# Kernel optimization log

Hardware: AMD Instinct MI355X
Metric: run time of the kernel (lower is better)

Reference implementation:

```python
import jax, jax.numpy as jnp
import numpy as np

B, T, I, H = 32, 1024, 512, 512


def _uniform(key, shape, stdv):
    return jax.random.uniform(key, shape, jnp.float32, -stdv, stdv)


def setup_inputs() -> dict:
    key = jax.random.key(0)
    ks = jax.random.split(key, 13)
    stdv = 1.0 / np.sqrt(H)
    return {
        "z": jax.random.normal(ks[0], (B, T, I, 2), jnp.float32),
        "W_zi": _uniform(ks[1], (I, H, 2), stdv), "W_hi": _uniform(ks[2], (H, H, 2), stdv), "b_i": _uniform(ks[3], (H,), stdv),
        "W_zf": _uniform(ks[4], (I, H, 2), stdv), "W_hf": _uniform(ks[5], (H, H, 2), stdv), "b_f": _uniform(ks[6], (H,), stdv),
        "W_zc": _uniform(ks[7], (I, H, 2), stdv), "W_hc": _uniform(ks[8], (H, H, 2), stdv), "b_c": _uniform(ks[9], (H, 2), stdv),
        "W_zo": _uniform(ks[10], (I, H, 2), stdv), "W_ho": _uniform(ks[11], (H, H, 2), stdv), "b_o": _uniform(ks[12], (H,), stdv),
    }


def complex_tanh(zr, zi):
    mag = jnp.maximum(jnp.sqrt(zr * zr + zi * zi + 1e-14), 1e-8)
    t = jnp.tanh(mag)
    return t * (zr / mag), t * (zi / mag)


def reference(z, W_zi, W_hi, b_i, W_zf, W_hf, b_f, W_zc, W_hc, b_c, W_zo, W_ho, b_o):
    zr, zi = z[..., 0], z[..., 1]  # (B,T,I)

    def in_proj_real(Wz):  # real part of complex matmul z @ Wz
        return jnp.einsum('bti,ih->bth', zr, Wz[..., 0]) - jnp.einsum('bti,ih->bth', zi, Wz[..., 1])

    xi = in_proj_real(W_zi)
    xf = in_proj_real(W_zf)
    xo = in_proj_real(W_zo)
    xcr = in_proj_real(W_zc)
    xci = jnp.einsum('bti,ih->bth', zi, W_zc[..., 0]) + jnp.einsum('bti,ih->bth', zr, W_zc[..., 1])

    # time-major for scan: (T,B,H)
    xs = tuple(jnp.swapaxes(a, 0, 1) for a in (xi, xf, xo, xcr, xci))

    def step(carry, x):
        h_r, h_i, c_r, c_i = carry
        xi_t, xf_t, xo_t, xcr_t, xci_t = x
        i_t = jax.nn.sigmoid(xi_t + h_r @ W_hi[..., 0] - h_i @ W_hi[..., 1] + b_i)
        f_t = jax.nn.sigmoid(xf_t + h_r @ W_hf[..., 0] - h_i @ W_hf[..., 1] + b_f)
        o_t = jax.nn.sigmoid(xo_t + h_r @ W_ho[..., 0] - h_i @ W_ho[..., 1] + b_o)
        cr = xcr_t + h_r @ W_hc[..., 0] - h_i @ W_hc[..., 1] + b_c[..., 0]
        ci = xci_t + h_i @ W_hc[..., 0] + h_r @ W_hc[..., 1] + b_c[..., 1]
        ctr, cti = complex_tanh(cr, ci)
        c_r = f_t * c_r + i_t * ctr
        c_i = f_t * c_i + i_t * cti
        hr, hi = complex_tanh(c_r, c_i)
        h_r = o_t * hr
        h_i = o_t * hi
        return (h_r, h_i, c_r, c_i), jnp.stack((h_r, h_i), axis=-1)

    zero = jnp.zeros((z.shape[0], W_hi.shape[0]), z.dtype)
    (h_r, h_i, c_r, c_i), hs = jax.lax.scan(step, (zero, zero, zero, zero), xs)
    hidden_seq = jnp.swapaxes(hs, 0, 1)  # (B,T,H,2)
    h_t = jnp.stack((h_r, h_i), axis=-1)
    c_t = jnp.stack((c_r, c_i), axis=-1)
    return hidden_seq, (h_t, c_t)
```

## Files before the change

### kernel.cpp

```cpp
#include <hip/hip_runtime.h>


#define B_ 32
#define T_ 1024
#define Hd 512
#define Kd 1024
#define Nd 2560
#define Md 32768
#define HS_ELEMS 33554432ull

typedef __attribute__((ext_vector_type(8))) short bf16x8;
typedef __attribute__((ext_vector_type(4))) float f32x4;

__device__ __forceinline__ unsigned short f_bf(float f) {
  unsigned int x; __builtin_memcpy(&x, &f, 4);
  unsigned int r = (x + 0x7FFFu + ((x >> 16) & 1u)) >> 16;
  return (unsigned short)r;
}
__device__ __forceinline__ float bf_f(unsigned short u) {
  unsigned int i = ((unsigned int)u) << 16; float f; __builtin_memcpy(&f, &i, 4); return f;
}
__device__ __forceinline__ float fsig(float x) { return 1.0f / (1.0f + __expf(-x)); }
__device__ __forceinline__ void ctanh_(float zr, float zi, float& tr, float& ti) {
  float m2 = zr * zr + zi * zi + 1e-14f;
  float mag = __fsqrt_rn(m2);
  float e = __expf(2.0f * mag);
  float th = 1.0f - 2.0f / (e + 1.0f);
  float s = th / mag;
  tr = zr * s; ti = zi * s;
}

__device__ __forceinline__ void gl16(const unsigned short* g, unsigned short* l) {
  __builtin_amdgcn_global_load_lds(
      (const __attribute__((address_space(1))) void*)g,
      (__attribute__((address_space(3))) void*)l, 16, 0, 0);
}

__device__ __forceinline__ unsigned int ald(const unsigned int* p) {
  return __hip_atomic_load(p, __ATOMIC_RELAXED, __HIP_MEMORY_SCOPE_AGENT);
}
__device__ __forceinline__ void ast(unsigned int* p, unsigned int v) {
  __hip_atomic_store(p, v, __ATOMIC_RELAXED, __HIP_MEMORY_SCOPE_AGENT);
}

__global__ void build_weights(const float* Wzi, const float* Whi, const float* bi,
                              const float* Wzf, const float* Whf, const float* bfv,
                              const float* Wzc, const float* Whc, const float* bc,
                              const float* Wzo, const float* Who, const float* bo,
                              unsigned short* WzT, unsigned short* WhT, float* bcomb) {
  int n = blockIdx.x;
  int slab = n / 80, wi = n % 80, g = wi / 16, hh = slab * 16 + (wi & 15);
  const float *Wz, *Wh;
  if (g == 0)      { Wz = Wzi; Wh = Whi; }
  else if (g == 1) { Wz = Wzf; Wh = Whf; }
  else if (g == 2) { Wz = Wzo; Wh = Who; }
  else             { Wz = Wzc; Wh = Whc; }
  int q0, q1; float s0, s1;
  if (g < 4) { q0 = 0; s0 = 1.f; q1 = 1; s1 = -1.f; }
  else       { q0 = 1; s0 = 1.f; q1 = 0; s1 =  1.f; }
  for (int k = threadIdx.x; k < Kd; k += 256) {
    int j = k >> 1, p = k & 1;
    int q = p ? q1 : q0; float sg = p ? s1 : s0;
    WzT[(size_t)n * Kd + k] = f_bf(sg * Wz[(j * Hd + hh) * 2 + q]);
    WhT[(size_t)n * Kd + k] = f_bf(sg * Wh[(j * Hd + hh) * 2 + q]);
  }
  if (threadIdx.x == 0) {
    float bv;
    if (g == 0) bv = bi[hh]; else if (g == 1) bv = bfv[hh];
    else if (g == 2) bv = bo[hh];
    else if (g == 3) bv = bc[2 * hh]; else bv = bc[2 * hh + 1];
    bcomb[n] = bv;
  }
}

__global__ void cvt_z(const float4* __restrict__ z, ushort4* __restrict__ Z2) {
  for (size_t i = (size_t)blockIdx.x * 256 + threadIdx.x; i < 8388608ull; i += 8192ull * 256) {
    float4 v = z[i];
    ushort4 o;
    o.x = f_bf(v.x); o.y = f_bf(v.y); o.z = f_bf(v.z); o.w = f_bf(v.w);
    Z2[i] = o;
  }
}

__global__ __launch_bounds__(256) void gemm_x(const unsigned short* __restrict__ Z2,
                                              const unsigned short* __restrict__ WT,
                                              unsigned short* __restrict__ X) {
  __shared__ unsigned short As[128 * 64];
  __shared__ unsigned short Bs[128 * 64];
  int tid = threadIdx.x, lane = tid & 63, wv = tid >> 6;
  int bid = blockIdx.x;
  int mb = bid / (Nd / 128), nb = bid % (Nd / 128);
  size_t m0 = (size_t)mb * 128, n0 = (size_t)nb * 128;
  int wr = wv >> 1, wc = wv & 1;
  int l15 = lane & 15, kg = lane >> 4;
  int lrow = tid >> 3;
  int lcol = (tid & 7) * 8;
  f32x4 acc[4][4] = {};
  for (int k0 = 0; k0 < Kd; k0 += 64) {
    __syncthreads();
#pragma unroll
    for (int c = 0; c < 4; ++c) {
      gl16(Z2 + (m0 + c * 32 + lrow) * Kd + k0 + lcol,
           As + (size_t)c * 2048 + wv * 512);
      gl16(WT + (n0 + c * 32 + lrow) * Kd + k0 + lcol,
           Bs + (size_t)c * 2048 + wv * 512);
    }
    __syncthreads();
#pragma unroll
    for (int ks = 0; ks < 2; ++ks) {
      int kk = ks * 32 + kg * 8;
      bf16x8 a[4], b[4];
#pragma unroll
      for (int i = 0; i < 4; ++i)
        a[i] = *reinterpret_cast<const bf16x8*>(&As[(wr * 64 + i * 16 + l15) * 64 + kk]);
#pragma unroll
      for (int j = 0; j < 4; ++j)
        b[j] = *reinterpret_cast<const bf16x8*>(&Bs[(wc * 64 + j * 16 + l15) * 64 + kk]);
#pragma unroll
      for (int i = 0; i < 4; ++i)
#pragma unroll
        for (int j = 0; j < 4; ++j)
          acc[i][j] = __builtin_amdgcn_mfma_f32_16x16x32_bf16(a[i], b[j], acc[i][j], 0, 0, 0);
    }
  }
#pragma unroll
  for (int i = 0; i < 4; ++i)
#pragma unroll
    for (int j = 0; j < 4; ++j) {
      size_t gm = m0 + wr * 64 + i * 16 + kg * 4;
      size_t gn = n0 + wc * 64 + j * 16 + l15;
#pragma unroll
      for (int r = 0; r < 4; ++r)
        X[(gm + r) * Nd + gn] = f_bf(acc[i][j][r]);
    }
}

#define CHUNK 8
#define STEPB (Nd * 2)
__global__ __launch_bounds__(512) void lstm_all(
    const unsigned short* __restrict__ WhT, const unsigned short* __restrict__ X,
    const float* __restrict__ bcomb, unsigned short* __restrict__ hb,
    int* __restrict__ flags, float* __restrict__ out) {
  __shared__ unsigned short Xs[2][CHUNK * STEPB / 2];
  __shared__ float xch[8][5][256];
  const int s = blockIdx.x;
  const int tid = threadIdx.x;
  const int wv = tid >> 6, lane = tid & 63;
  const int kh = wv >> 1, mh = wv & 1;
  const int l15 = lane & 15, kg = lane >> 4;
  const int cb = tid >> 4;
  const int ch = tid & 15;
  const int hh = s * 16 + ch;

  auto stage = [&](int tbase, int buf) {
#pragma unroll
    for (int j = 0; j < 5; ++j) {
      unsigned int P = (unsigned int)(wv * 5 + j) * 1024u + (unsigned int)lane * 16u;
      unsigned int st = P / STEPB, r = P % STEPB;
      unsigned int b = r / 160u, rem = r % 160u;
      gl16(X + ((size_t)b * T_ + (tbase + st)) * Nd + s * 80 + rem / 2,
           &Xs[buf][(size_t)(wv * 5 + j) * 512]);
    }
  };
  stage(0, 0);

  bf16x8 w[5][8];
#pragma unroll
  for (int g = 0; g < 5; ++g)
#pragma unroll
    for (int ks = 0; ks < 8; ++ks)
      w[g][ks] = *reinterpret_cast<const bf16x8*>(
          &WhT[(size_t)(s * 80 + g * 16 + l15) * Kd + kh * 256 + ks * 32 + kg * 8]);

  float bias[5];
#pragma unroll
  for (int g = 0; g < 5; ++g) bias[g] = bcomb[s * 80 + g * 16 + ch];
  float cr = 0.f, ci = 0.f;

  ast((unsigned int*)hb + (size_t)cb * 512 + s * 16 + ch, 0u);
  asm volatile("s_waitcnt vmcnt(0)" ::: "memory");
  __syncthreads();
  if (tid == 0) ast((unsigned int*)&flags[s], 1u);

  const int fidx = kh * 8 + (lane & 7);
  const int mb = cb >> 4;
  const int xidx = ((cb & 15) >> 2) * 64 + ch * 4 + (cb & 3);

  for (int t = 0; t < T_; ++t) {
    const unsigned int need = (unsigned int)(t + 1);
    while (true) {
      unsigned int v = ald((const unsigned int*)&flags[fidx]);
      if (__all(v >= need)) break;
    }
    asm volatile("" ::: "memory");

    const unsigned short* hin = hb + (size_t)(t % 3) * 32768;
    unsigned long long hpa = (unsigned long long)(
        hin + (size_t)(mh * 16 + l15) * Kd + kh * 256 + kg * 8);
    bf16x8 a[8];
#define HL(i, off) asm volatile("global_load_dwordx4 %0, %1, off offset:" #off " sc0 sc1" \
                                 : "=v"(a[i]) : "v"(hpa) : "memory")
    HL(0, 0); HL(1, 64); HL(2, 128); HL(3, 192);
    HL(4, 256); HL(5, 320); HL(6, 384); HL(7, 448);
#undef HL
    asm volatile("s_waitcnt vmcnt(0)" ::: "memory");
    __builtin_amdgcn_sched_barrier(0);

    if ((t & (CHUNK - 1)) == 0 && t + CHUNK < T_)
      stage(t + CHUNK, ((t >> 3) + 1) & 1);

    f32x4 acc[5] = {};
#pragma unroll
    for (int ks = 0; ks < 8; ++ks)
#pragma unroll
      for (int g = 0; g < 5; ++g)
        acc[g] = __builtin_amdgcn_mfma_f32_16x16x32_bf16(a[ks], w[g][ks], acc[g], 0, 0, 0);

#pragma unroll
    for (int g = 0; g < 5; ++g)
      *reinterpret_cast<f32x4*>(&xch[wv][g][lane * 4]) = acc[g];
    __syncthreads();

    const unsigned short* xsl = &Xs[(t >> 3) & 1][(t & 7) * Nd + cb * 80 + ch];
    float pre[5];
#pragma unroll
    for (int g = 0; g < 5; ++g) {
      float p = bias[g] + bf_f(xsl[g * 16]);
#pragma unroll
      for (int q = 0; q < 4; ++q) p += xch[q * 2 + mb][g][xidx];
      pre[g] = p;
    }
    float ig = fsig(pre[0]), fg = fsig(pre[1]), og = fsig(pre[2]);
    float ctr, cti; ctanh_(pre[3], pre[4], ctr, cti);
    cr = fg * cr + ig * ctr;
    ci = fg * ci + ig * cti;
    float hr0, hi0; ctanh_(cr, ci, hr0, hi0);
    float hr = og * hr0, hi = og * hi0;

    unsigned short* hnext = hb + (size_t)((t + 1) % 3) * 32768;
    unsigned int hv = (unsigned int)f_bf(hr) | ((unsigned int)f_bf(hi) << 16);
    ast((unsigned int*)hnext + (size_t)cb * 512 + s * 16 + ch, hv);
    if (t < T_ - 1) {
      asm volatile("s_waitcnt vmcnt(0)" ::: "memory");
      __syncthreads();
      if (tid == 0) ast((unsigned int*)&flags[s], (unsigned int)(t + 2));
    }

    size_t oidx = ((size_t)cb * T_ + t) * (Hd * 2) + hh * 2;
    *reinterpret_cast<float2*>(&out[oidx]) = make_float2(hr, hi);
    if (t == T_ - 1) {
      size_t fb = HS_ELEMS + ((size_t)cb * Hd + hh) * 2;
      *reinterpret_cast<float2*>(&out[fb]) = make_float2(hr, hi);
      *reinterpret_cast<float2*>(&out[fb + 32768ull]) = make_float2(cr, ci);
    }
  }
}

extern "C" void kernel_launch(void* const* d_in, const int* in_sizes, int n_in,
                              void* d_out, int out_size, void* d_ws, size_t ws_size,
                              hipStream_t stream) {
  const float* z   = (const float*)d_in[0];
  const float* Wzi = (const float*)d_in[1];
  const float* Whi = (const float*)d_in[2];
  const float* bi  = (const float*)d_in[3];
  const float* Wzf = (const float*)d_in[4];
  const float* Whf = (const float*)d_in[5];
  const float* bfv = (const float*)d_in[6];
  const float* Wzc = (const float*)d_in[7];
  const float* Whc = (const float*)d_in[8];
  const float* bc  = (const float*)d_in[9];
  const float* Wzo = (const float*)d_in[10];
  const float* Who = (const float*)d_in[11];
  const float* bo  = (const float*)d_in[12];
  float* out = (float*)d_out;

  size_t off = 0;
  char* ws = (char*)d_ws;
  auto take = [&](size_t nbytes) {
    void* p = ws + off; off += (nbytes + 255) & ~(size_t)255; return p;
  };
  unsigned short* WzT  = (unsigned short*)take((size_t)Nd * Kd * 2);
  unsigned short* WhT  = (unsigned short*)take((size_t)Nd * Kd * 2);
  float*          bcmb = (float*)take(Nd * 4);
  unsigned short* Z2   = (unsigned short*)take((size_t)Md * Kd * 2);
  unsigned short* X    = (unsigned short*)take((size_t)Md * Nd * 2);
  unsigned short* hb   = (unsigned short*)take(3 * 32768 * 2);
  int*            flags = (int*)take(64 * 4);

  hipMemsetAsync(flags, 0, 64 * 4, stream);
  build_weights<<<Nd, 256, 0, stream>>>(Wzi, Whi, bi, Wzf, Whf, bfv,
                                        Wzc, Whc, bc, Wzo, Who, bo,
                                        WzT, WhT, bcmb);
  cvt_z<<<8192, 256, 0, stream>>>((const float4*)z, (ushort4*)Z2);
  gemm_x<<<(Md / 128) * (Nd / 128), 256, 0, stream>>>(Z2, WzT, X);
  lstm_all<<<32, 512, 0, stream>>>(WhT, X, bcmb, hb, flags, out);
}
```

Baseline: 5.164 ms.

## Use per-wave flags for inter-block step sync and batch output stores

Replaces the per-block flag (set after a block-wide barrier) with per-wave flags, so each wave publishes its slice of h as soon as its own stores complete. Consumers poll only the 32 flags covering the h rows they read. Output stores are buffered in registers and written every 8 steps, and the X staging load is issued after the step computation. This shortens the serial critical path of the recurrent loop but adds more flag polling traffic and register pressure.

```diff
diff --git a/kernel.cpp b/kernel.cpp
--- a/kernel.cpp
+++ b/kernel.cpp
@@ -140,7 +140,7 @@
 __global__ __launch_bounds__(512) void lstm_all(
     const unsigned short* __restrict__ WhT, const unsigned short* __restrict__ X,
     const float* __restrict__ bcomb, unsigned short* __restrict__ hb,
-    int* __restrict__ flags, float* __restrict__ out) {
+    int* __restrict__ ctl, float* __restrict__ out) {
   __shared__ unsigned short Xs[2][CHUNK * STEPB / 2];
   __shared__ float xch[8][5][256];
   const int s = blockIdx.x;
@@ -152,6 +152,12 @@
   const int ch = tid & 15;
   const int hh = s * 16 + ch;
 
+  unsigned int* flags2 = (unsigned int*)(ctl + 16);
+  unsigned int* hbu = (unsigned int*)hb;
+  const int pidx = ((s >> 3) * 2 + (wv >> 2)) * 32 + (s & 7) * 4 + (wv & 3);
+  const int fbase = (kh * 2 + mh) * 32;
+  const int i32 = lane & 31;
+
   auto stage = [&](int tbase, int buf) {
 #pragma unroll
     for (int j = 0; j < 5; ++j) {
@@ -177,81 +183,88 @@
   for (int g = 0; g < 5; ++g) bias[g] = bcomb[s * 80 + g * 16 + ch];
   float cr = 0.f, ci = 0.f;
 
-  ast((unsigned int*)hb + (size_t)cb * 512 + s * 16 + ch, 0u);
+  ast(hbu + (size_t)cb * 512 + hh, 0u);
   asm volatile("s_waitcnt vmcnt(0)" ::: "memory");
-  __syncthreads();
-  if (tid == 0) ast((unsigned int*)&flags[s], 1u);
-
-  const int fidx = kh * 8 + (lane & 7);
+  if (lane == 0) ast(&flags2[pidx], 1u);
+
   const int mb = cb >> 4;
   const int xidx = ((cb & 15) >> 2) * 64 + ch * 4 + (cb & 3);
 
-  for (int t = 0; t < T_; ++t) {
-    const unsigned int need = (unsigned int)(t + 1);
-    while (true) {
-      unsigned int v = ald((const unsigned int*)&flags[fidx]);
-      if (__all(v >= need)) break;
-    }
-    asm volatile("" ::: "memory");
-
-    const unsigned short* hin = hb + (size_t)(t % 3) * 32768;
-    unsigned long long hpa = (unsigned long long)(
-        hin + (size_t)(mh * 16 + l15) * Kd + kh * 256 + kg * 8);
-    bf16x8 a[8];
+  float2 hist[8];
+
+  for (int tb = 0; tb < T_; tb += 8) {
+#pragma unroll
+    for (int j = 0; j < 8; ++j) {
+      const int t = tb + j;
+      const unsigned int need = (unsigned int)(t + 1);
+      while (true) {
+        unsigned int v = ald(&flags2[fbase + i32]);
+        if (__all(v >= need)) break;
+      }
+      asm volatile("" ::: "memory");
+
+      const unsigned short* hin = hb + (size_t)(t % 3) * 32768;
+      unsigned long long hpa = (unsigned long long)(
+          hin + (size_t)(mh * 16 + l15) * Kd + kh * 256 + kg * 8);
+      bf16x8 a[8];
 #define HL(i, off) asm volatile("global_load_dwordx4 %0, %1, off offset:" #off " sc0 sc1" \
                                  : "=v"(a[i]) : "v"(hpa) : "memory")
-    HL(0, 0); HL(1, 64); HL(2, 128); HL(3, 192);
-    HL(4, 256); HL(5, 320); HL(6, 384); HL(7, 448);
+      HL(0, 0); HL(1, 64); HL(2, 128); HL(3, 192);
+      HL(4, 256); HL(5, 320); HL(6, 384); HL(7, 448);
 #undef HL
-    asm volatile("s_waitcnt vmcnt(0)" ::: "memory");
-    __builtin_amdgcn_sched_barrier(0);
-
-    if ((t & (CHUNK - 1)) == 0 && t + CHUNK < T_)
-      stage(t + CHUNK, ((t >> 3) + 1) & 1);
-
-    f32x4 acc[5] = {};
-#pragma unroll
-    for (int ks = 0; ks < 8; ++ks)
+      asm volatile("s_waitcnt vmcnt(0)" ::: "memory");
+      __builtin_amdgcn_sched_barrier(0);
+
+      f32x4 acc[5] = {};
+#pragma unroll
+      for (int ks = 0; ks < 8; ++ks)
+#pragma unroll
+        for (int g = 0; g < 5; ++g)
+          acc[g] = __builtin_amdgcn_mfma_f32_16x16x32_bf16(a[ks], w[g][ks], acc[g], 0, 0, 0);
+
 #pragma unroll
       for (int g = 0; g < 5; ++g)
-        acc[g] = __builtin_amdgcn_mfma_f32_16x16x32_bf16(a[ks], w[g][ks], acc[g], 0, 0, 0);
-
-#pragma unroll
-    for (int g = 0; g < 5; ++g)
-      *reinterpret_cast<f32x4*>(&xch[wv][g][lane * 4]) = acc[g];
-    __syncthreads();
-
-    const unsigned short* xsl = &Xs[(t >> 3) & 1][(t & 7) * Nd + cb * 80 + ch];
-    float pre[5];
-#pragma unroll
-    for (int g = 0; g < 5; ++g) {
-      float p = bias[g] + bf_f(xsl[g * 16]);
-#pragma unroll
-      for (int q = 0; q < 4; ++q) p += xch[q * 2 + mb][g][xidx];
-      pre[g] = p;
-    }
-    float ig = fsig(pre[0]), fg = fsig(pre[1]), og = fsig(pre[2]);
-    float ctr, cti; ctanh_(pre[3], pre[4], ctr, cti);
-    cr = fg * cr + ig * ctr;
-    ci = fg * ci + ig * cti;
-    float hr0, hi0; ctanh_(cr, ci, hr0, hi0);
-    float hr = og * hr0, hi = og * hi0;
-
-    unsigned short* hnext = hb + (size_t)((t + 1) % 3) * 32768;
-    unsigned int hv = (unsigned int)f_bf(hr) | ((unsigned int)f_bf(hi) << 16);
-    ast((unsigned int*)hnext + (size_t)cb * 512 + s * 16 + ch, hv);
-    if (t < T_ - 1) {
-      asm volatile("s_waitcnt vmcnt(0)" ::: "memory");
+        *reinterpret_cast<f32x4*>(&xch[wv][g][lane * 4]) = acc[g];
       __syncthreads();
-      if (tid == 0) ast((unsigned int*)&flags[s], (unsigned int)(t + 2));
-    }
-
-    size_t oidx = ((size_t)cb * T_ + t) * (Hd * 2) + hh * 2;
-    *reinterpret_cast<float2*>(&out[oidx]) = make_float2(hr, hi);
-    if (t == T_ - 1) {
-      size_t fb = HS_ELEMS + ((size_t)cb * Hd + hh) * 2;
-      *reinterpret_cast<float2*>(&out[fb]) = make_float2(hr, hi);
-      *reinterpret_cast<float2*>(&out[fb + 32768ull]) = make_float2(cr, ci);
+
+      const unsigned short* xsl = &Xs[(t >> 3) & 1][(t & 7) * Nd + cb * 80 + ch];
+      float pre[5];
+#pragma unroll
+      for (int g = 0; g < 5; ++g) {
+        float p = bias[g] + bf_f(xsl[g * 16]);
+#pragma unroll
+        for (int q = 0; q < 4; ++q) p += xch[q * 2 + mb][g][xidx];
+        pre[g] = p;
+      }
+      float ig = fsig(pre[0]), fg = fsig(pre[1]), og = fsig(pre[2]);
+      float ctr, cti; ctanh_(pre[3], pre[4], ctr, cti);
+      cr = fg * cr + ig * ctr;
+      ci = fg * ci + ig * cti;
+      float hr0, hi0; ctanh_(cr, ci, hr0, hi0);
+      float hr = og * hr0, hi = og * hi0;
+      hist[j] = make_float2(hr, hi);
+
+      unsigned int hv = (unsigned int)f_bf(hr) | ((unsigned int)f_bf(hi) << 16);
+      ast(hbu + (size_t)((t + 1) % 3) * 16384 + (size_t)cb * 512 + hh, hv);
+      if (t < T_ - 1) {
+        asm volatile("s_waitcnt vmcnt(0)" ::: "memory");
+        if (lane == 0) ast(&flags2[pidx], (unsigned int)(t + 2));
+      }
+
+      if (j == 7) {
+#pragma unroll
+        for (int q = 0; q < 8; ++q) {
+          size_t oidx = ((size_t)cb * T_ + (t - 7 + q)) * (Hd * 2) + hh * 2;
+          *reinterpret_cast<float2*>(&out[oidx]) = hist[q];
+        }
+      }
+      if (j == 0 && t + 8 < T_) stage(t + 8, ((t >> 3) + 1) & 1);
+      if (t == T_ - 1) {
+        size_t fb = HS_ELEMS + ((size_t)cb * Hd + hh) * 2;
+        *reinterpret_cast<float2*>(&out[fb]) = make_float2(hr, hi);
+        *reinterpret_cast<float2*>(&out[fb + 32768ull]) = make_float2(cr, ci);
+      }
+      __syncthreads();
     }
   }
 }
@@ -285,13 +298,13 @@
   unsigned short* Z2   = (unsigned short*)take((size_t)Md * Kd * 2);
   unsigned short* X    = (unsigned short*)take((size_t)Md * Nd * 2);
   unsigned short* hb   = (unsigned short*)take(3 * 32768 * 2);
-  int*            flags = (int*)take(64 * 4);
-
-  hipMemsetAsync(flags, 0, 64 * 4, stream);
+  int*            ctl  = (int*)take(4096);
+
+  hipMemsetAsync(ctl, 0, 4096, stream);
   build_weights<<<Nd, 256, 0, stream>>>(Wzi, Whi, bi, Wzf, Whf, bfv,
                                         Wzc, Whc, bc, Wzo, Who, bo,
                                         WzT, WhT, bcmb);
   cvt_z<<<8192, 256, 0, stream>>>((const float4*)z, (ushort4*)Z2);
   gemm_x<<<(Md / 128) * (Nd / 128), 256, 0, stream>>>(Z2, WzT, X);
-  lstm_all<<<32, 512, 0, stream>>>(WhT, X, bcmb, hb, flags, out);
-}
+  lstm_all<<<32, 512, 0, stream>>>(WhT, X, bcmb, hb, ctl, out);
+}
```

After: 5.792 ms. 1.12x slower.
